# Kernel tuning notes

Measured on AMD Instinct MI355X. Metric: run time of the kernel, lower is better.

## Reference

```python
import jax, jax.numpy as jnp
import numpy as np

NUM_HEADS = 12
NUM_BLOCKS = 12
EPS = 1e-5


def _layernorm(x, g, b):
    mu = jnp.mean(x, axis=-1, keepdims=True)
    var = jnp.mean(jnp.square(x - mu), axis=-1, keepdims=True)
    return (x - mu) * jax.lax.rsqrt(var + EPS) * g + b


def setup_inputs() -> dict:
    key = jax.random.key(0)
    ks = jax.random.split(key, 16)
    B, N, D, F = 4, 512, 768, 3072
    s = 1.0 / np.sqrt(D)
    sf = 1.0 / np.sqrt(F)
    return {
        "x": jax.random.normal(ks[0], (B, N, D), jnp.float32),
        "Wq": jax.random.normal(ks[1], (D, D), jnp.float32) * s,
        "bq": jnp.zeros((D,), jnp.float32),
        "Wk": jax.random.normal(ks[2], (D, D), jnp.float32) * s,
        "bk": jnp.zeros((D,), jnp.float32),
        "Wv": jax.random.normal(ks[3], (D, D), jnp.float32) * s,
        "bv": jnp.zeros((D,), jnp.float32),
        "g1": jnp.ones((D,), jnp.float32),
        "be1": jnp.zeros((D,), jnp.float32),
        "g2": jnp.ones((D,), jnp.float32),
        "be2": jnp.zeros((D,), jnp.float32),
        "W0": jax.random.normal(ks[4], (D, F), jnp.float32) * s,
        "b0": jnp.zeros((F,), jnp.float32),
        "W1": jax.random.normal(ks[5], (F, D), jnp.float32) * sf,
        "b1": jnp.zeros((D,), jnp.float32),
    }


def _attention(x, Wq, bq, Wk, bk, Wv, bv):
    B, N, D = x.shape
    H = NUM_HEADS
    hd = D // H
    q = (x @ Wq + bq).reshape(B, N, H, hd)
    k = (x @ Wk + bk).reshape(B, N, H, hd)
    v = (x @ Wv + bv).reshape(B, N, H, hd)
    # scores: [B, H, N, N], scaled by 1/sqrt(head_dim)
    scores = jnp.einsum("bqhd,bkhd->bhqk", q, k) / np.sqrt(hd)
    weights = jax.nn.softmax(scores, axis=-1)
    out = jnp.einsum("bhqk,bkhd->bqhd", weights, v)
    return out.reshape(B, N, D)


def reference(x, Wq, bq, Wk, bk, Wv, bv, g1, be1, g2, be2, W0, b0, W1, b1):
    # All blocks share the same weights (module appends the same block instance).
    for _ in range(NUM_BLOCKS):
        x = x + _attention(_layernorm(x, g1, be1), Wq, bq, Wk, bk, Wv, bv)
        h = _layernorm(x, g2, be2)
        h = jax.nn.gelu(h @ W0 + b0, approximate=False) @ W1 + b1
        x = x + h
    return x
```

## Files before the change

### kernel.cpp

```cpp
#include <hip/hip_runtime.h>
#include <stdint.h>

typedef float  f32x4  __attribute__((ext_vector_type(4)));
typedef __bf16 bf16x8 __attribute__((ext_vector_type(8)));
typedef short  s16x8  __attribute__((ext_vector_type(8)));

#define DEV __device__ __forceinline__

DEV short f2b(float f) {
    union { float f; unsigned u; } c; c.f = f;
    unsigned u = c.u;
    unsigned r = (u + 0x7fffu + ((u >> 16) & 1u)) >> 16;
    return (short)r;
}
DEV float b2f(short s) {
    union { unsigned u; float f; } c; c.u = ((unsigned)(unsigned short)s) << 16;
    return c.f;
}

DEV void gload_lds16(const void* g, void* l) {
    __builtin_amdgcn_global_load_lds(
        (const __attribute__((address_space(1))) void*)g,
        (__attribute__((address_space(3))) void*)l, 16, 0, 0);
}

template<int BM, int BN, int MODE, int NSPLIT>
__global__ __launch_bounds__(256) void gemm_bt(
    const short* __restrict__ A, const short* __restrict__ Bt,
    const float* __restrict__ bias,
    float* __restrict__ outf, short* __restrict__ outs0,
    short* __restrict__ outs1, short* __restrict__ outs2,
    long sA, long sB, long sO, int M, int N, int K)
{
    constexpr int BK = 64;
    constexpr int FM = BM / 32, FN = BN / 32;
    static_assert((BM + BN) / 32 == 4, "vmcnt(4) assumes 4 loads per stage");
    __shared__ __align__(16) short As[3][BM * BK];
    __shared__ __align__(16) short Bs[3][BN * BK];

    const int tid  = threadIdx.x;
    const int w    = tid >> 6, lane = tid & 63;
    const int wr   = w >> 1,  wc   = w & 1;
    const int l16  = lane & 15, lhi = lane >> 4, sw = lane & 7;

    const int gx   = gridDim.x;
    const int nwg  = gx * gridDim.y;
    const int flat = blockIdx.y * gx + blockIdx.x;
    const int nf   = (flat & 7) * (nwg >> 3) + (flat >> 3);
    const int bx   = nf % gx, by = nf / gx;

    int z, kz;
    if constexpr (NSPLIT > 1) { z = 0; kz = blockIdx.z; }
    else                      { z = blockIdx.z; kz = 0; }

    const short* Ab = A  + (long)z * sA + (long)by * BM * K;
    const short* Bb = Bt + (long)z * sB + (long)bx * BN * K;

    const int ktPer = (K >> 6) / NSPLIT;
    const int ktBeg = kz * ktPer, ktEnd = ktBeg + ktPer;

    f32x4 acc[FM][FN];
#pragma unroll
    for (int m = 0; m < FM; ++m)
#pragma unroll
        for (int n = 0; n < FN; ++n) acc[m][n] = (f32x4)(0.0f);

    auto stage = [&](int buf, int kt) {
        const short* Ag = Ab + kt * BK;
#pragma unroll
        for (int i = 0; i < BM / 32; ++i) {
            int seg = i * 256 + tid;
            int row = seg >> 3;
            int gcs = (tid & 7) ^ (row & 7);
            gload_lds16(Ag + (long)row * K + gcs * 8, &As[buf][(i * 256 + w * 64) * 8]);
        }
        const short* Bg = Bb + kt * BK;
#pragma unroll
        for (int i = 0; i < BN / 32; ++i) {
            int seg = i * 256 + tid;
            int row = seg >> 3;
            int gcs = (tid & 7) ^ (row & 7);
            gload_lds16(Bg + (long)row * K + gcs * 8, &Bs[buf][(i * 256 + w * 64) * 8]);
        }
    };

    stage(0, ktBeg);
    stage(1, ktBeg + 1);
    asm volatile("s_waitcnt vmcnt(4)" ::: "memory");
    __builtin_amdgcn_s_barrier();

    int cur = 0;
    for (int kt = ktBeg; kt < ktEnd; ++kt) {
        const bool more = (kt + 2 < ktEnd);
        if (more) stage(cur >= 1 ? cur - 1 : cur + 2, kt + 2);

        const short* Ac = &As[cur][0];
        const short* Bc = &Bs[cur][0];
#pragma unroll
        for (int kk = 0; kk < 2; ++kk) {
            bf16x8 af[FM], bfr[FN];
#pragma unroll
            for (int m = 0; m < FM; ++m) {
                int ar = wr * (BM / 2) + m * 16 + l16;
                int ks = (kk * 4 + lhi) ^ sw;
                af[m] = *(const bf16x8*)(Ac + ar * BK + ks * 8);
            }
#pragma unroll
            for (int n = 0; n < FN; ++n) {
                int br = wc * (BN / 2) + n * 16 + l16;
                int ks = (kk * 4 + lhi) ^ sw;
                bfr[n] = *(const bf16x8*)(Bc + br * BK + ks * 8);
            }
#pragma unroll
            for (int m = 0; m < FM; ++m)
#pragma unroll
                for (int n = 0; n < FN; ++n)
                    acc[m][n] = __builtin_amdgcn_mfma_f32_16x16x32_bf16(
                        af[m], bfr[n], acc[m][n], 0, 0, 0);
        }
        if (more) asm volatile("s_waitcnt vmcnt(4)" ::: "memory");
        else      asm volatile("s_waitcnt vmcnt(0)" ::: "memory");
        __builtin_amdgcn_s_barrier();
        cur = (cur + 1 == 3) ? 0 : cur + 1;
    }

    const int m0 = by * BM, n0 = bx * BN;
#pragma unroll
    for (int m = 0; m < FM; ++m) {
#pragma unroll
        for (int n = 0; n < FN; ++n) {
            const int grow0 = m0 + wr * (BM / 2) + m * 16 + lhi * 4;
            const int gcol  = n0 + wc * (BN / 2) + n * 16 + l16;
#pragma unroll
            for (int r = 0; r < 4; ++r) {
                float val = acc[m][n][r];
                int grow = grow0 + r;
                if constexpr (MODE == 1) {
                    float v = val + bias[gcol];
                    int d  = gcol & 63;
                    int hh = gcol >> 6;
                    int bb = grow >> 9, s = grow & 511;
                    if (hh < 12) {
                        outs0[((long)((bb * 12 + hh) * 512 + s) << 6) + d] = f2b(v * 0.125f);
                    } else if (hh < 24) {
                        outs1[((long)((bb * 12 + (hh - 12)) * 512 + s) << 6) + d] = f2b(v);
                    } else {
                        outs2[((long)((bb * 12 + (hh - 24)) * 64 + d) << 9) + s] = f2b(v);
                    }
                } else if constexpr (MODE == 2) {
                    float v = val + bias[gcol];
                    v = 0.5f * v * (1.0f + erff(v * 0.70710678118f));
                    outs0[(long)grow * N + gcol] = f2b(v);
                } else {
                    outf[(long)kz * M * N + (long)grow * N + gcol] = val;
                }
            }
        }
    }
}

template<int DO_LN>
__global__ __launch_bounds__(256) void ffn2_reduce_ln(
    const float* __restrict__ part, const float* __restrict__ bias,
    float* __restrict__ x, const float* __restrict__ g,
    const float* __restrict__ be, short* __restrict__ out)
{
    int row  = blockIdx.x * 4 + (threadIdx.x >> 6);
    int lane = threadIdx.x & 63;
    const float4* p0 = (const float4*)part + (long)row * 192;
    const float4* p1 = (const float4*)(part + 2048l * 768) + (long)row * 192;
    const float4* b4 = (const float4*)bias;
    float4* xr = (float4*)(x + (long)row * 768);

    float f[12];
#pragma unroll
    for (int jb = 0; jb < 3; ++jb) {
        int idx = lane + 64 * jb;
        float4 a = p0[idx], b = p1[idx], c = b4[idx], xv = xr[idx];
        xv.x += a.x + b.x + c.x;
        xv.y += a.y + b.y + c.y;
        xv.z += a.z + b.z + c.z;
        xv.w += a.w + b.w + c.w;
        xr[idx] = xv;
        f[4 * jb + 0] = xv.x; f[4 * jb + 1] = xv.y;
        f[4 * jb + 2] = xv.z; f[4 * jb + 3] = xv.w;
    }

    if constexpr (DO_LN) {
        float s = 0.f;
#pragma unroll
        for (int j = 0; j < 12; ++j) s += f[j];
#pragma unroll
        for (int o = 32; o; o >>= 1) s += __shfl_xor(s, o);
        float mu = s * (1.0f / 768.0f);
        float s2 = 0.f;
#pragma unroll
        for (int j = 0; j < 12; ++j) { f[j] -= mu; s2 += f[j] * f[j]; }
#pragma unroll
        for (int o = 32; o; o >>= 1) s2 += __shfl_xor(s2, o);
        float rstd = rsqrtf(s2 * (1.0f / 768.0f) + 1e-5f);

        const float4* gr = (const float4*)g;
        const float4* br = (const float4*)be;
        short4* orow = (short4*)(out + (long)row * 768);
#pragma unroll
        for (int jb = 0; jb < 3; ++jb) {
            float4 gg = gr[lane + 64 * jb], bb = br[lane + 64 * jb];
            short4 o4;
            o4.x = f2b(f[4 * jb + 0] * rstd * gg.x + bb.x);
            o4.y = f2b(f[4 * jb + 1] * rstd * gg.y + bb.y);
            o4.z = f2b(f[4 * jb + 2] * rstd * gg.z + bb.z);
            o4.w = f2b(f[4 * jb + 3] * rstd * gg.w + bb.w);
            orow[lane + 64 * jb] = o4;
        }
    }
}

__global__ __launch_bounds__(256) void attn_fused(
    const short* __restrict__ Qg,
    const short* __restrict__ Kg,
    const short* __restrict__ VTg,
    float* __restrict__ x)
{
    __shared__ __align__(16) short Qs[64 * 64];
    __shared__ __align__(16) short Ks[2][64 * 64];
    __shared__ __align__(16) short Vs[2][64 * 64];
    __shared__ __align__(16) short Ps[4][16 * 64];

    const int tid = threadIdx.x;
    const int w = tid >> 6, lane = tid & 63;
    const int l16 = lane & 15, lhi = lane >> 4;

    const int f  = blockIdx.y * 8 + blockIdx.x;
    const int nf = (f & 7) * 48 + (f >> 3);
    const int z  = nf >> 3, qt = nf & 7;
    const int q0 = qt * 64;

    const short* Qb = Qg  + (long)z * 512 * 64 + q0 * 64;
    const short* Kb = Kg  + (long)z * 512 * 64;
    const short* Vb = VTg + (long)z * 64 * 512;

    auto stageQ = [&]() {
#pragma unroll
        for (int i = 0; i < 2; ++i) {
            int seg = i * 256 + tid;
            int row = seg >> 3;
            int gc  = (seg & 7) ^ (row & 7);
            gload_lds16(Qb + row * 64 + gc * 8, Qs + (i * 256 + w * 64) * 8);
        }
    };
    auto stageK = [&](int buf, int kt) {
#pragma unroll
        for (int i = 0; i < 2; ++i) {
            int seg = i * 256 + tid;
            int row = seg >> 3;
            int gc  = (seg & 7) ^ (row & 7);
            gload_lds16(Kb + (kt * 64 + row) * 64 + gc * 8, &Ks[buf][(i * 256 + w * 64) * 8]);
        }
    };
    auto stageV = [&](int buf, int kt) {
#pragma unroll
        for (int i = 0; i < 2; ++i) {
            int seg = i * 256 + tid;
            int row = seg >> 3;
            int gc  = (seg & 7) ^ (row & 7);
            gload_lds16(Vb + (long)row * 512 + kt * 64 + gc * 8, &Vs[buf][(i * 256 + w * 64) * 8]);
        }
    };

    stageQ(); stageK(0, 0); stageV(0, 0);
    asm volatile("s_waitcnt vmcnt(0)" ::: "memory");
    __syncthreads();

    bf16x8 bq[2];
    {
        int qr = w * 16 + l16;
#pragma unroll
        for (int kk = 0; kk < 2; ++kk)
            bq[kk] = *(const bf16x8*)(Qs + qr * 64 + (((kk * 4 + lhi) ^ (l16 & 7)) * 8));
    }

    float m = -3e38f, l = 0.0f;
    f32x4 acc[4];
#pragma unroll
    for (int bn = 0; bn < 4; ++bn) acc[bn] = (f32x4)(0.0f);

    int cur = 0;
    for (int kt = 0; kt < 8; ++kt) {
        if (kt < 7) { stageK(cur ^ 1, kt + 1); stageV(cur ^ 1, kt + 1); }

        f32x4 s[4];
#pragma unroll
        for (int km = 0; km < 4; ++km) s[km] = (f32x4)(0.0f);
#pragma unroll
        for (int kk = 0; kk < 2; ++kk) {
#pragma unroll
            for (int km = 0; km < 4; ++km) {
                int kr = km * 16 + l16;
                bf16x8 ak = *(const bf16x8*)(&Ks[cur][kr * 64 + (((kk * 4 + lhi) ^ (l16 & 7)) * 8)]);
                s[km] = __builtin_amdgcn_mfma_f32_16x16x32_bf16(ak, bq[kk], s[km], 0, 0, 0);
            }
        }

        float tmax = -3e38f;
#pragma unroll
        for (int km = 0; km < 4; ++km)
#pragma unroll
            for (int r = 0; r < 4; ++r) tmax = fmaxf(tmax, s[km][r]);
        tmax = fmaxf(tmax, __shfl_xor(tmax, 16));
        tmax = fmaxf(tmax, __shfl_xor(tmax, 32));
        float mn = fmaxf(m, tmax);
        float sc = __expf(m - mn);
        float p[16];
        float ts = 0.0f;
#pragma unroll
        for (int km = 0; km < 4; ++km)
#pragma unroll
            for (int r = 0; r < 4; ++r) {
                float e = __expf(s[km][r] - mn);
                p[km * 4 + r] = e; ts += e;
            }
        ts += __shfl_xor(ts, 16);
        ts += __shfl_xor(ts, 32);
        l = l * sc + ts; m = mn;

        float scr[4];
#pragma unroll
        for (int r = 0; r < 4; ++r) scr[r] = __shfl(sc, lhi * 4 + r);
#pragma unroll
        for (int bn = 0; bn < 4; ++bn)
#pragma unroll
            for (int r = 0; r < 4; ++r) acc[bn][r] *= scr[r];

        {
            short* Pw = &Ps[w][0];
#pragma unroll
            for (int km = 0; km < 4; ++km)
#pragma unroll
                for (int r = 0; r < 4; ++r) {
                    int k = km * 16 + lhi * 4 + r;
                    int g = k >> 3, e = k & 7;
                    Pw[l16 * 64 + ((g ^ (l16 & 7)) * 8) + e] = f2b(p[km * 4 + r]);
                }
        }

#pragma unroll
        for (int kk = 0; kk < 2; ++kk) {
            bf16x8 ap = *(const bf16x8*)(&Ps[w][l16 * 64 + (((kk * 4 + lhi) ^ (l16 & 7)) * 8)]);
#pragma unroll
            for (int bn = 0; bn < 4; ++bn) {
                int vr = bn * 16 + l16;
                bf16x8 bv = *(const bf16x8*)(&Vs[cur][vr * 64 + (((kk * 4 + lhi) ^ (l16 & 7)) * 8)]);
                acc[bn] = __builtin_amdgcn_mfma_f32_16x16x32_bf16(ap, bv, acc[bn], 0, 0, 0);
            }
        }

        asm volatile("s_waitcnt vmcnt(0)" ::: "memory");
        __builtin_amdgcn_s_barrier();
        cur ^= 1;
    }

    float inv = 1.0f / l;
    float invr[4];
#pragma unroll
    for (int r = 0; r < 4; ++r) invr[r] = __shfl(inv, lhi * 4 + r);
    const int zb = z / 12, zh = z - (z / 12) * 12;
#pragma unroll
    for (int bn = 0; bn < 4; ++bn)
#pragma unroll
        for (int r = 0; r < 4; ++r) {
            long idx = ((long)(zb * 512 + q0 + w * 16 + lhi * 4 + r)) * 768 + zh * 64 + bn * 16 + l16;
            x[idx] += acc[bn][r] * invr[r];
        }
}

__global__ __launch_bounds__(256) void ln_kernel(
    const float* __restrict__ x, const float* __restrict__ g,
    const float* __restrict__ be, short* __restrict__ out)
{
    int row  = blockIdx.x * 4 + (threadIdx.x >> 6);
    int lane = threadIdx.x & 63;
    const float4* xr = (const float4*)(x + (long)row * 768);
    float4 v0 = xr[lane], v1 = xr[lane + 64], v2 = xr[lane + 128];
    float f[12] = {v0.x, v0.y, v0.z, v0.w, v1.x, v1.y, v1.z, v1.w, v2.x, v2.y, v2.z, v2.w};

    float s = 0.f;
#pragma unroll
    for (int j = 0; j < 12; ++j) s += f[j];
#pragma unroll
    for (int o = 32; o; o >>= 1) s += __shfl_xor(s, o);
    float mu = s * (1.0f / 768.0f);
    float s2 = 0.f;
#pragma unroll
    for (int j = 0; j < 12; ++j) { f[j] -= mu; s2 += f[j] * f[j]; }
#pragma unroll
    for (int o = 32; o; o >>= 1) s2 += __shfl_xor(s2, o);
    float rstd = rsqrtf(s2 * (1.0f / 768.0f) + 1e-5f);

    const float4* gr = (const float4*)g;
    const float4* br = (const float4*)be;
    short4* orow = (short4*)(out + (long)row * 768);
#pragma unroll
    for (int jb = 0; jb < 3; ++jb) {
        float4 gg = gr[lane + 64 * jb], bb = br[lane + 64 * jb];
        short4 o4;
        o4.x = f2b(f[4 * jb + 0] * rstd * gg.x + bb.x);
        o4.y = f2b(f[4 * jb + 1] * rstd * gg.y + bb.y);
        o4.z = f2b(f[4 * jb + 2] * rstd * gg.z + bb.z);
        o4.w = f2b(f[4 * jb + 3] * rstd * gg.w + bb.w);
        orow[lane + 64 * jb] = o4;
    }
}

__global__ __launch_bounds__(256) void transpose_w(
    const float* __restrict__ in, short* __restrict__ out, int R, int C)
{
    __shared__ float t[32][33];
    int r0 = blockIdx.y * 32, c0 = blockIdx.x * 32;
    int tx = threadIdx.x & 31, ty = threadIdx.x >> 5;
#pragma unroll
    for (int p = 0; p < 4; ++p)
        t[ty + 8 * p][tx] = in[(long)(r0 + ty + 8 * p) * C + c0 + tx];
    __syncthreads();
#pragma unroll
    for (int p = 0; p < 4; ++p)
        out[(long)(c0 + ty + 8 * p) * R + r0 + tx] = f2b(t[tx][ty + 8 * p]);
}

__global__ void concat_bias(const float* __restrict__ bq, const float* __restrict__ bk,
                            const float* __restrict__ bv, float* __restrict__ o)
{
    int i = blockIdx.x * 256 + threadIdx.x;
    if (i < 768) { o[i] = bq[i]; o[768 + i] = bk[i]; o[1536 + i] = bv[i]; }
}

extern "C" void kernel_launch(void* const* d_in, const int* in_sizes, int n_in,
                              void* d_out, int out_size, void* d_ws, size_t ws_size,
                              hipStream_t stream)
{
    (void)in_sizes; (void)n_in; (void)out_size; (void)ws_size;
    const float* x_in = (const float*)d_in[0];
    const float* Wq  = (const float*)d_in[1];
    const float* bq  = (const float*)d_in[2];
    const float* Wk  = (const float*)d_in[3];
    const float* bk  = (const float*)d_in[4];
    const float* Wv  = (const float*)d_in[5];
    const float* bv  = (const float*)d_in[6];
    const float* g1  = (const float*)d_in[7];
    const float* be1 = (const float*)d_in[8];
    const float* g2  = (const float*)d_in[9];
    const float* be2 = (const float*)d_in[10];
    const float* W0  = (const float*)d_in[11];
    const float* b0  = (const float*)d_in[12];
    const float* W1  = (const float*)d_in[13];
    const float* b1  = (const float*)d_in[14];

    float* x = (float*)d_out;

    char* ws = (char*)d_ws;
    size_t off = 0;
    auto alloc = [&](size_t bytes) -> char* {
        char* p = ws + off; off = (off + bytes + 255) & ~(size_t)255; return p;
    };
    short* wqkvt = (short*)alloc(2304l * 768 * 2);
    short* w0t   = (short*)alloc(3072l * 768 * 2);
    short* w1t   = (short*)alloc(768l * 3072 * 2);
    float* bqkv  = (float*)alloc(2304 * 4);
    short* lnb   = (short*)alloc(2048l * 768 * 2);
    short* q     = (short*)alloc(2048l * 768 * 2);
    short* k     = (short*)alloc(2048l * 768 * 2);
    short* vt    = (short*)alloc(2048l * 768 * 2);
    short* h     = (short*)alloc(2048l * 3072 * 2);
    float* part  = (float*)alloc(2l * 2048 * 768 * 4);

    hipMemcpyAsync(x, x_in, 2048l * 768 * 4, hipMemcpyDeviceToDevice, stream);

    transpose_w<<<dim3(24, 24), 256, 0, stream>>>(Wq, wqkvt, 768, 768);
    transpose_w<<<dim3(24, 24), 256, 0, stream>>>(Wk, wqkvt + 768l * 768, 768, 768);
    transpose_w<<<dim3(24, 24), 256, 0, stream>>>(Wv, wqkvt + 2l * 768 * 768, 768, 768);
    transpose_w<<<dim3(96, 24), 256, 0, stream>>>(W0, w0t, 768, 3072);
    transpose_w<<<dim3(24, 96), 256, 0, stream>>>(W1, w1t, 3072, 768);
    concat_bias<<<3, 256, 0, stream>>>(bq, bk, bv, bqkv);

    for (int it = 0; it < 12; ++it) {
        if (it == 0)
            ln_kernel<<<512, 256, 0, stream>>>(x, g1, be1, lnb);
        gemm_bt<64, 64, 1, 1><<<dim3(36, 32, 1), 256, 0, stream>>>(
            lnb, wqkvt, bqkv, nullptr, q, k, vt, 0, 0, 0, 2048, 2304, 768);
        attn_fused<<<dim3(8, 48), 256, 0, stream>>>(q, k, vt, x);
        ln_kernel<<<512, 256, 0, stream>>>(x, g2, be2, lnb);
        gemm_bt<64, 64, 2, 1><<<dim3(48, 32, 1), 256, 0, stream>>>(
            lnb, w0t, b0, nullptr, h, nullptr, nullptr, 0, 0, 0, 2048, 3072, 768);
        gemm_bt<64, 64, 3, 2><<<dim3(12, 32, 2), 256, 0, stream>>>(
            h, w1t, nullptr, part, nullptr, nullptr, nullptr, 0, 0, 0, 2048, 768, 3072);
        if (it < 11)
            ffn2_reduce_ln<1><<<512, 256, 0, stream>>>(part, b1, x, g1, be1, lnb);
        else
            ffn2_reduce_ln<0><<<512, 256, 0, stream>>>(part, b1, x, nullptr, nullptr, nullptr);
    }
}
```

Baseline: 1.165 ms.

## Switch GEMMs to 128x128 tiles with double buffering

Moves the GEMM kernels from 64x64 tiles to 128x128 tiles, quadrupling per-wave MFMA work and raising operand reuse from LDS. The LDS pipeline drops from three stages to two to keep shared memory in budget, and the waits become vmcnt(0). The grids shrink to 288, 384 and 192 workgroups, which is near or below the CU count on MI355X (256 CUs) and cuts occupancy and latency hiding. The shallower prefetch may also expose more global-load latency.

```diff
diff --git a/kernel.cpp b/kernel.cpp
--- a/kernel.cpp
+++ b/kernel.cpp
@@ -25,18 +25,17 @@
 }
 
 template<int BM, int BN, int MODE, int NSPLIT>
-__global__ __launch_bounds__(256) void gemm_bt(
+DEV void gemm_body(
     const short* __restrict__ A, const short* __restrict__ Bt,
     const float* __restrict__ bias,
     float* __restrict__ outf, short* __restrict__ outs0,
     short* __restrict__ outs1, short* __restrict__ outs2,
-    long sA, long sB, long sO, int M, int N, int K)
+    long sA, long sB, int M, int N, int K)
 {
     constexpr int BK = 64;
     constexpr int FM = BM / 32, FN = BN / 32;
-    static_assert((BM + BN) / 32 == 4, "vmcnt(4) assumes 4 loads per stage");
-    __shared__ __align__(16) short As[3][BM * BK];
-    __shared__ __align__(16) short Bs[3][BN * BK];
+    __shared__ __align__(16) short As[2][BM * BK];
+    __shared__ __align__(16) short Bs[2][BN * BK];
 
     const int tid  = threadIdx.x;
     const int w    = tid >> 6, lane = tid & 63;
@@ -85,15 +84,12 @@
     };
 
     stage(0, ktBeg);
-    stage(1, ktBeg + 1);
-    asm volatile("s_waitcnt vmcnt(4)" ::: "memory");
+    asm volatile("s_waitcnt vmcnt(0)" ::: "memory");
     __builtin_amdgcn_s_barrier();
 
     int cur = 0;
     for (int kt = ktBeg; kt < ktEnd; ++kt) {
-        const bool more = (kt + 2 < ktEnd);
-        if (more) stage(cur >= 1 ? cur - 1 : cur + 2, kt + 2);
-
+        if (kt + 1 < ktEnd) stage(cur ^ 1, kt + 1);
         const short* Ac = &As[cur][0];
         const short* Bc = &Bs[cur][0];
 #pragma unroll
@@ -118,10 +114,9 @@
                     acc[m][n] = __builtin_amdgcn_mfma_f32_16x16x32_bf16(
                         af[m], bfr[n], acc[m][n], 0, 0, 0);
         }
-        if (more) asm volatile("s_waitcnt vmcnt(4)" ::: "memory");
-        else      asm volatile("s_waitcnt vmcnt(0)" ::: "memory");
+        asm volatile("s_waitcnt vmcnt(0)" ::: "memory");
         __builtin_amdgcn_s_barrier();
-        cur = (cur + 1 == 3) ? 0 : cur + 1;
+        cur ^= 1;
     }
 
     const int m0 = by * BM, n0 = bx * BN;
@@ -159,6 +154,23 @@
     }
 }
 
+__global__ __launch_bounds__(256) void gemm_qkv(
+    const short* A, const short* Bt, const float* bias,
+    short* q, short* k, short* vt)
+{
+    gemm_body<128, 128, 1, 1>(A, Bt, bias, nullptr, q, k, vt, 0, 0, 2048, 2304, 768);
+}
+__global__ __launch_bounds__(256) void gemm_ffn1(
+    const short* A, const short* Bt, const float* bias, short* h)
+{
+    gemm_body<128, 128, 2, 1>(A, Bt, bias, nullptr, h, nullptr, nullptr, 0, 0, 2048, 3072, 768);
+}
+__global__ __launch_bounds__(256) void gemm_ffn2(
+    const short* A, const short* Bt, float* part)
+{
+    gemm_body<128, 128, 3, 2>(A, Bt, nullptr, part, nullptr, nullptr, nullptr, 0, 0, 2048, 768, 3072);
+}
+
 template<int DO_LN>
 __global__ __launch_bounds__(256) void ffn2_reduce_ln(
     const float* __restrict__ part, const float* __restrict__ bias,
@@ -485,14 +497,11 @@
     for (int it = 0; it < 12; ++it) {
         if (it == 0)
             ln_kernel<<<512, 256, 0, stream>>>(x, g1, be1, lnb);
-        gemm_bt<64, 64, 1, 1><<<dim3(36, 32, 1), 256, 0, stream>>>(
-            lnb, wqkvt, bqkv, nullptr, q, k, vt, 0, 0, 0, 2048, 2304, 768);
+        gemm_qkv<<<dim3(18, 16), 256, 0, stream>>>(lnb, wqkvt, bqkv, q, k, vt);
         attn_fused<<<dim3(8, 48), 256, 0, stream>>>(q, k, vt, x);
         ln_kernel<<<512, 256, 0, stream>>>(x, g2, be2, lnb);
-        gemm_bt<64, 64, 2, 1><<<dim3(48, 32, 1), 256, 0, stream>>>(
-            lnb, w0t, b0, nullptr, h, nullptr, nullptr, 0, 0, 0, 2048, 3072, 768);
-        gemm_bt<64, 64, 3, 2><<<dim3(12, 32, 2), 256, 0, stream>>>(
-            h, w1t, nullptr, part, nullptr, nullptr, nullptr, 0, 0, 0, 2048, 768, 3072);
+        gemm_ffn1<<<dim3(24, 16), 256, 0, stream>>>(lnb, w0t, b0, h);
+        gemm_ffn2<<<dim3(6, 16, 2), 256, 0, stream>>>(h, w1t, part);
         if (it < 11)
             ffn2_reduce_ln<1><<<512, 256, 0, stream>>>(part, b1, x, g1, be1, lnb);
         else
```

New measurement: 1.253 ms. +7.6%, slower.
